# Optimization experiments

Measured on AMD Instinct MI355X. Metric: run time of the kernel, lower is better.

## Reference

```python
import jax, jax.numpy as jnp
import numpy as np

N_NODES = 100000
HIDDEN = 512
NUM_GRAPHS = 1024


def setup_inputs() -> dict:
    key = jax.random.key(0)
    k_h, k_b, k_w1, k_w2 = jax.random.split(key, 4)
    s1 = 1.0 / np.sqrt(HIDDEN)
    return {
        "h": jax.random.normal(k_h, (N_NODES, HIDDEN), dtype=jnp.float32),
        "batch_vec": jnp.sort(jax.random.randint(k_b, (N_NODES,), 0, NUM_GRAPHS, dtype=jnp.int32)),
        "W1": jax.random.normal(k_w1, (HIDDEN, HIDDEN), dtype=jnp.float32) * s1,
        "b1": jnp.zeros((HIDDEN,), dtype=jnp.float32),
        "W2": jax.random.normal(k_w2, (HIDDEN, 1), dtype=jnp.float32) * s1,
        "b2": jnp.zeros((1,), dtype=jnp.float32),
    }


def reference(h, batch_vec, W1, b1, W2, b2):
    # gate MLP (Dropout is identity in eval): [N, hidden] -> [N]
    gate = (jax.nn.gelu(h @ W1 + b1, approximate=False) @ W2 + b2)[:, 0]
    # segment softmax over graphs (batch_vec)
    m = jax.ops.segment_max(gate, batch_vec, num_segments=NUM_GRAPHS)
    e = jnp.exp(gate - m[batch_vec])
    denom = jax.ops.segment_sum(e, batch_vec, num_segments=NUM_GRAPHS)
    alpha = e / denom[batch_vec]  # [N]
    # scatter-weighted sum: [num_graphs, hidden]
    return jax.ops.segment_sum(alpha[:, None] * h, batch_vec, num_segments=NUM_GRAPHS)
```

## Files before the change

### kernel.cpp

```cpp
#include <hip/hip_runtime.h>
#include <hip/hip_bf16.h>
#include <float.h>

#define N_NODES 100000
#define HID     512
#define NGRAPH  1024
#define BM      48
#define NBLK    ((N_NODES + BM - 1) / BM)

typedef __bf16 bf16_t;
typedef bf16_t bf16x8 __attribute__((ext_vector_type(8)));
typedef float  f32x4  __attribute__((ext_vector_type(4)));

__device__ __forceinline__ float fast_gelu(float x) {
    const float z = __builtin_fabsf(x) * 0.70710678118654752f;
    const float t = __fdividef(1.0f, __builtin_fmaf(0.3275911f, z, 1.0f));
    float p = __builtin_fmaf(1.061405429f, t, -1.453152027f);
    p = __builtin_fmaf(p, t, 1.421413741f);
    p = __builtin_fmaf(p, t, -0.284496736f);
    p = __builtin_fmaf(p, t, 0.254829592f);
    p *= t;
    const float e    = __expf(-z * z);
    const float erfz = __builtin_fmaf(-p, e, 1.0f);
    const float s    = __builtin_copysignf(erfz, x);
    return 0.5f * x * (1.0f + s);
}

__global__ void __launch_bounds__(256) k_w1t_tiled(const float* __restrict__ w1,
                                                   bf16_t* __restrict__ bt) {
    const int u   = blockIdx.x * 256 + threadIdx.x;
    const int col = u & 511;
    const int g4  = u >> 9;
    const int k0  = g4 * 8;
    bf16x8 v;
    #pragma unroll
    for (int e = 0; e < 8; ++e)
        v[e] = (bf16_t)w1[(size_t)(k0 + e) * HID + col];
    *reinterpret_cast<bf16x8*>(bt + (size_t)u * 8) = v;
}

__global__ void __launch_bounds__(1024, 8) k_gemm_gate(const float* __restrict__ h,
                                                       const bf16_t* __restrict__ bt,
                                                       const float* __restrict__ b1,
                                                       const float* __restrict__ w2,
                                                       const float* __restrict__ b2,
                                                       float* __restrict__ gate) {
    __shared__ __align__(16) bf16_t As[BM * HID];
    __shared__ float gp[16][BM];

    const int tid  = threadIdx.x;
    const int lane = tid & 63;
    const int wv   = tid >> 6;
    const int l15  = lane & 15;
    const int l4   = lane >> 4;

    const int brow = blockIdx.x * BM;

    #pragma unroll
    for (int i = 0; i < 3; ++i) {
        const int idx = i * 1024 + tid;
        const int row = idx >> 6;
        const int cu  = idx & 63;
        const int grow = brow + row;
        f32x4 s0 = f32x4{0.f, 0.f, 0.f, 0.f}, s1 = s0;
        if (grow < N_NODES) {
            const f32x4* p = reinterpret_cast<const f32x4*>(
                h + (size_t)grow * HID + cu * 8);
            s0 = p[0];
            s1 = p[1];
        }
        bf16x8 v;
        #pragma unroll
        for (int j = 0; j < 4; ++j) { v[j] = (bf16_t)s0[j]; v[4 + j] = (bf16_t)s1[j]; }
        *reinterpret_cast<bf16x8*>(
            (char*)As + row * 1024 + ((cu ^ (row & 7)) * 16)) = v;
    }
    __syncthreads();

    const bf16_t* bbase = bt + ((size_t)l4 * 512 + wv * 32 + l15) * 8;
    const char*   abase = (const char*)As + l15 * 1024;
    f32x4 acc[3][2] = {};
    #pragma unroll 2
    for (int kt = 0; kt < 16; ++kt) {
        bf16x8 bfr[2];
        #pragma unroll
        for (int nf = 0; nf < 2; ++nf)
            bfr[nf] = *reinterpret_cast<const bf16x8*>(
                bbase + (size_t)kt * 16384 + nf * 128);
        const int chunkoff = ((kt * 4 + l4) ^ (l15 & 7)) * 16;
        bf16x8 af[3];
        #pragma unroll
        for (int mf = 0; mf < 3; ++mf)
            af[mf] = *reinterpret_cast<const bf16x8*>(abase + mf * 16384 + chunkoff);
        #pragma unroll
        for (int mf = 0; mf < 3; ++mf)
            #pragma unroll
            for (int nf = 0; nf < 2; ++nf)
                acc[mf][nf] = __builtin_amdgcn_mfma_f32_16x16x32_bf16(
                    af[mf], bfr[nf], acc[mf][nf], 0, 0, 0);
    }

    float pr[12];
    #pragma unroll
    for (int i = 0; i < 12; ++i) pr[i] = 0.f;
    #pragma unroll
    for (int nf = 0; nf < 2; ++nf) {
        const int cg    = wv * 32 + nf * 16 + l15;
        const float b1v = b1[cg];
        const float w2v = w2[cg];
        #pragma unroll
        for (int mf = 0; mf < 3; ++mf) {
            #pragma unroll
            for (int rr = 0; rr < 4; ++rr) {
                const float ge = fast_gelu(acc[mf][nf][rr] + b1v);
                pr[mf * 4 + rr] = fmaf(ge, w2v, pr[mf * 4 + rr]);
            }
        }
    }
    #pragma unroll
    for (int i = 0; i < 12; ++i) {
        float v = pr[i];
        v += __shfl_xor(v, 1);
        v += __shfl_xor(v, 2);
        v += __shfl_xor(v, 4);
        v += __shfl_xor(v, 8);
        pr[i] = v;
    }
    if (l15 == 0) {
        #pragma unroll
        for (int mf = 0; mf < 3; ++mf)
            #pragma unroll
            for (int rr = 0; rr < 4; ++rr)
                gp[wv][mf * 16 + l4 * 4 + rr] = pr[mf * 4 + rr];
    }
    __syncthreads();
    if (tid < BM) {
        const int grow = brow + tid;
        if (grow < N_NODES) {
            float s = b2[0];
            #pragma unroll
            for (int w = 0; w < 16; ++w) s += gp[w][tid];
            gate[grow] = s;
        }
    }
}

__global__ void __launch_bounds__(256) k_pool(const float* __restrict__ h,
                                              const int* __restrict__ bv,
                                              const float* __restrict__ gate,
                                              float* __restrict__ out) {
    const int g   = blockIdx.x;
    const int tid = threadIdx.x;
    __shared__ int   s_bounds[2];
    __shared__ float s_red[4];
    __shared__ float s_alpha[256];

    if (tid == 0) {
        int lo = 0, hi = N_NODES;
        while (lo < hi) { int mid = (lo + hi) >> 1; if (bv[mid] < g) lo = mid + 1; else hi = mid; }
        s_bounds[0] = lo;
        int lo2 = lo, hi2 = N_NODES;
        while (lo2 < hi2) { int mid = (lo2 + hi2) >> 1; if (bv[mid] < g + 1) lo2 = mid + 1; else hi2 = mid; }
        s_bounds[1] = lo2;
    }
    __syncthreads();
    const int start = s_bounds[0], end = s_bounds[1];

    float2 acc = make_float2(0.f, 0.f);
    if (start < end) {
        const int lane = tid & 63, wv = tid >> 6;
        float lm = -FLT_MAX;
        for (int i = start + tid; i < end; i += 256) lm = fmaxf(lm, gate[i]);
        #pragma unroll
        for (int o = 32; o; o >>= 1) lm = fmaxf(lm, __shfl_xor(lm, o));
        if (lane == 0) s_red[wv] = lm;
        __syncthreads();
        const float m = fmaxf(fmaxf(s_red[0], s_red[1]), fmaxf(s_red[2], s_red[3]));
        __syncthreads();
        float ls = 0.f;
        for (int i = start + tid; i < end; i += 256) ls += expf(gate[i] - m);
        #pragma unroll
        for (int o = 32; o; o >>= 1) ls += __shfl_xor(ls, o);
        if (lane == 0) s_red[wv] = ls;
        __syncthreads();
        const float inv = 1.f / (s_red[0] + s_red[1] + s_red[2] + s_red[3]);
        const float* hcol = h + tid * 2;
        for (int base = start; base < end; base += 256) {
            const int j = base + tid;
            const float av = (j < end) ? expf(gate[j] - m) * inv : 0.f;
            __syncthreads();
            s_alpha[tid] = av;
            __syncthreads();
            const int cnt = min(256, end - base);
            for (int jj = 0; jj < cnt; ++jj) {
                const float a = s_alpha[jj];
                const float2 hv = *reinterpret_cast<const float2*>(
                    hcol + (size_t)(base + jj) * HID);
                acc.x = fmaf(a, hv.x, acc.x);
                acc.y = fmaf(a, hv.y, acc.y);
            }
        }
    }
    *reinterpret_cast<float2*>(out + (size_t)g * HID + tid * 2) = acc;
}

extern "C" void kernel_launch(void* const* d_in, const int* in_sizes, int n_in,
                              void* d_out, int out_size, void* d_ws, size_t ws_size,
                              hipStream_t stream) {
    const float* h  = (const float*)d_in[0];
    const int*   bv = (const int*)d_in[1];
    const float* W1 = (const float*)d_in[2];
    const float* b1 = (const float*)d_in[3];
    const float* W2 = (const float*)d_in[4];
    const float* b2 = (const float*)d_in[5];
    float* out = (float*)d_out;

    char* ws = (char*)d_ws;
    bf16_t* bt   = (bf16_t*)ws;
    float*  gate = (float*)(ws + 524288);

    k_w1t_tiled<<<dim3(128), dim3(256), 0, stream>>>(W1, bt);
    k_gemm_gate<<<dim3(NBLK), dim3(1024), 0, stream>>>(h, bt, b1, W2, b2, gate);
    k_pool<<<dim3(NGRAPH), dim3(256), 0, stream>>>(h, bv, gate, out);
}
```

Measured before the change: 142.8 us.

## Make gate GEMM persistent with double-buffered LDS prefetch of next row block

The gate GEMM kernel now launches a fixed grid of 256 persistent blocks, each looping over row blocks. While computing the current block, it loads the next block of h into registers and writes it to a second LDS buffer, and it software-pipelines the W1 fragment loads two k-steps ahead. This aims to hide global-memory latency behind MFMA work and to drop the per-block startup cost. In exchange it doubles LDS use (two 48 KB buffers, so launch bounds drop to 4), raises register pressure, and with 256 blocks on the MI355X may leave CUs underfilled.

```diff
diff --git a/kernel.cpp b/kernel.cpp
--- a/kernel.cpp
+++ b/kernel.cpp
@@ -6,7 +6,8 @@
 #define HID     512
 #define NGRAPH  1024
 #define BM      48
-#define NBLK    ((N_NODES + BM - 1) / BM)
+#define NRB     ((N_NODES + BM - 1) / BM)
+#define GRID    256
 
 typedef __bf16 bf16_t;
 typedef bf16_t bf16x8 __attribute__((ext_vector_type(8)));
@@ -39,13 +40,13 @@
     *reinterpret_cast<bf16x8*>(bt + (size_t)u * 8) = v;
 }
 
-__global__ void __launch_bounds__(1024, 8) k_gemm_gate(const float* __restrict__ h,
+__global__ void __launch_bounds__(1024, 4) k_gemm_gate(const float* __restrict__ h,
                                                        const bf16_t* __restrict__ bt,
                                                        const float* __restrict__ b1,
                                                        const float* __restrict__ w2,
                                                        const float* __restrict__ b2,
                                                        float* __restrict__ gate) {
-    __shared__ __align__(16) bf16_t As[BM * HID];
+    __shared__ __align__(16) bf16_t As[2][BM * HID];
     __shared__ float gp[16][BM];
 
     const int tid  = threadIdx.x;
@@ -54,94 +55,150 @@
     const int l15  = lane & 15;
     const int l4   = lane >> 4;
 
-    const int brow = blockIdx.x * BM;
-
-    #pragma unroll
-    for (int i = 0; i < 3; ++i) {
-        const int idx = i * 1024 + tid;
-        const int row = idx >> 6;
-        const int cu  = idx & 63;
-        const int grow = brow + row;
-        f32x4 s0 = f32x4{0.f, 0.f, 0.f, 0.f}, s1 = s0;
-        if (grow < N_NODES) {
-            const f32x4* p = reinterpret_cast<const f32x4*>(
-                h + (size_t)grow * HID + cu * 8);
-            s0 = p[0];
-            s1 = p[1];
-        }
-        bf16x8 v;
-        #pragma unroll
-        for (int j = 0; j < 4; ++j) { v[j] = (bf16_t)s0[j]; v[4 + j] = (bf16_t)s1[j]; }
-        *reinterpret_cast<bf16x8*>(
-            (char*)As + row * 1024 + ((cu ^ (row & 7)) * 16)) = v;
-    }
-    __syncthreads();
-
-    const bf16_t* bbase = bt + ((size_t)l4 * 512 + wv * 32 + l15) * 8;
-    const char*   abase = (const char*)As + l15 * 1024;
-    f32x4 acc[3][2] = {};
-    #pragma unroll 2
-    for (int kt = 0; kt < 16; ++kt) {
-        bf16x8 bfr[2];
-        #pragma unroll
-        for (int nf = 0; nf < 2; ++nf)
-            bfr[nf] = *reinterpret_cast<const bf16x8*>(
-                bbase + (size_t)kt * 16384 + nf * 128);
-        const int chunkoff = ((kt * 4 + l4) ^ (l15 & 7)) * 16;
-        bf16x8 af[3];
-        #pragma unroll
-        for (int mf = 0; mf < 3; ++mf)
-            af[mf] = *reinterpret_cast<const bf16x8*>(abase + mf * 16384 + chunkoff);
-        #pragma unroll
-        for (int mf = 0; mf < 3; ++mf)
-            #pragma unroll
-            for (int nf = 0; nf < 2; ++nf)
-                acc[mf][nf] = __builtin_amdgcn_mfma_f32_16x16x32_bf16(
-                    af[mf], bfr[nf], acc[mf][nf], 0, 0, 0);
-    }
-
-    float pr[12];
-    #pragma unroll
-    for (int i = 0; i < 12; ++i) pr[i] = 0.f;
+    float b1v[2], w2v[2];
     #pragma unroll
     for (int nf = 0; nf < 2; ++nf) {
-        const int cg    = wv * 32 + nf * 16 + l15;
-        const float b1v = b1[cg];
-        const float w2v = w2[cg];
-        #pragma unroll
-        for (int mf = 0; mf < 3; ++mf) {
-            #pragma unroll
-            for (int rr = 0; rr < 4; ++rr) {
-                const float ge = fast_gelu(acc[mf][nf][rr] + b1v);
-                pr[mf * 4 + rr] = fmaf(ge, w2v, pr[mf * 4 + rr]);
-            }
-        }
-    }
-    #pragma unroll
-    for (int i = 0; i < 12; ++i) {
-        float v = pr[i];
-        v += __shfl_xor(v, 1);
-        v += __shfl_xor(v, 2);
-        v += __shfl_xor(v, 4);
-        v += __shfl_xor(v, 8);
-        pr[i] = v;
-    }
-    if (l15 == 0) {
-        #pragma unroll
-        for (int mf = 0; mf < 3; ++mf)
-            #pragma unroll
-            for (int rr = 0; rr < 4; ++rr)
-                gp[wv][mf * 16 + l4 * 4 + rr] = pr[mf * 4 + rr];
+        const int cg = wv * 32 + nf * 16 + l15;
+        b1v[nf] = b1[cg];
+        w2v[nf] = w2[cg];
+    }
+    const float b2v = b2[0];
+
+    const bf16_t* bbase = bt + ((size_t)l4 * 512 + wv * 32 + l15) * 8;
+
+    {
+        const int rb = blockIdx.x;
+        #pragma unroll
+        for (int i = 0; i < 3; ++i) {
+            const int idx = i * 1024 + tid;
+            const int row = idx >> 6;
+            const int cu  = idx & 63;
+            const int grow = rb * BM + row;
+            f32x4 s0 = f32x4{0.f, 0.f, 0.f, 0.f}, s1 = s0;
+            if (grow < N_NODES) {
+                const f32x4* p = reinterpret_cast<const f32x4*>(
+                    h + (size_t)grow * HID + cu * 8);
+                s0 = p[0]; s1 = p[1];
+            }
+            bf16x8 v;
+            #pragma unroll
+            for (int j = 0; j < 4; ++j) { v[j] = (bf16_t)s0[j]; v[4 + j] = (bf16_t)s1[j]; }
+            *reinterpret_cast<bf16x8*>(
+                (char*)&As[0][0] + row * 1024 + ((cu ^ (row & 7)) * 16)) = v;
+        }
     }
     __syncthreads();
-    if (tid < BM) {
-        const int grow = brow + tid;
-        if (grow < N_NODES) {
-            float s = b2[0];
-            #pragma unroll
-            for (int w = 0; w < 16; ++w) s += gp[w][tid];
-            gate[grow] = s;
-        }
+
+    int cur = 0;
+    for (int rb = blockIdx.x; rb < NRB; rb += GRID) {
+        const int  rbn  = rb + GRID;
+        const bool have = rbn < NRB;
+
+        f32x4 st[6];
+        if (have) {
+            #pragma unroll
+            for (int i = 0; i < 3; ++i) {
+                const int idx = i * 1024 + tid;
+                const int row = idx >> 6;
+                const int cu  = idx & 63;
+                const int grow = rbn * BM + row;
+                f32x4 s0 = f32x4{0.f, 0.f, 0.f, 0.f}, s1 = s0;
+                if (grow < N_NODES) {
+                    const f32x4* p = reinterpret_cast<const f32x4*>(
+                        h + (size_t)grow * HID + cu * 8);
+                    s0 = p[0]; s1 = p[1];
+                }
+                st[2 * i] = s0; st[2 * i + 1] = s1;
+            }
+        }
+
+        const char* abase = (const char*)&As[cur][0] + l15 * 1024;
+        f32x4 acc[3][2] = {};
+        bf16x8 breg[2][2];
+        #pragma unroll
+        for (int nf = 0; nf < 2; ++nf)
+            breg[0][nf] = *reinterpret_cast<const bf16x8*>(bbase + nf * 128);
+        #pragma unroll
+        for (int nf = 0; nf < 2; ++nf)
+            breg[1][nf] = *reinterpret_cast<const bf16x8*>(bbase + 16384 + nf * 128);
+        #pragma unroll 4
+        for (int kt = 0; kt < 16; ++kt) {
+            const int chunkoff = ((kt * 4 + l4) ^ (l15 & 7)) * 16;
+            bf16x8 af[3];
+            #pragma unroll
+            for (int mf = 0; mf < 3; ++mf)
+                af[mf] = *reinterpret_cast<const bf16x8*>(
+                    abase + mf * 16384 + chunkoff);
+            #pragma unroll
+            for (int mf = 0; mf < 3; ++mf)
+                #pragma unroll
+                for (int nf = 0; nf < 2; ++nf)
+                    acc[mf][nf] = __builtin_amdgcn_mfma_f32_16x16x32_bf16(
+                        af[mf], breg[kt & 1][nf], acc[mf][nf], 0, 0, 0);
+            if (kt < 14) {
+                #pragma unroll
+                for (int nf = 0; nf < 2; ++nf)
+                    breg[kt & 1][nf] = *reinterpret_cast<const bf16x8*>(
+                        bbase + (size_t)(kt + 2) * 16384 + nf * 128);
+            }
+        }
+
+        if (have) {
+            #pragma unroll
+            for (int i = 0; i < 3; ++i) {
+                const int idx = i * 1024 + tid;
+                const int row = idx >> 6;
+                const int cu  = idx & 63;
+                bf16x8 v;
+                #pragma unroll
+                for (int j = 0; j < 4; ++j) { v[j] = (bf16_t)st[2*i][j]; v[4+j] = (bf16_t)st[2*i+1][j]; }
+                *reinterpret_cast<bf16x8*>(
+                    (char*)&As[cur ^ 1][0] + row * 1024 + ((cu ^ (row & 7)) * 16)) = v;
+            }
+        }
+
+        float pr[12];
+        #pragma unroll
+        for (int i = 0; i < 12; ++i) pr[i] = 0.f;
+        #pragma unroll
+        for (int nf = 0; nf < 2; ++nf) {
+            #pragma unroll
+            for (int mf = 0; mf < 3; ++mf) {
+                #pragma unroll
+                for (int rr = 0; rr < 4; ++rr) {
+                    const float ge = fast_gelu(acc[mf][nf][rr] + b1v[nf]);
+                    pr[mf * 4 + rr] = fmaf(ge, w2v[nf], pr[mf * 4 + rr]);
+                }
+            }
+        }
+        #pragma unroll
+        for (int i = 0; i < 12; ++i) {
+            float v = pr[i];
+            v += __shfl_xor(v, 1);
+            v += __shfl_xor(v, 2);
+            v += __shfl_xor(v, 4);
+            v += __shfl_xor(v, 8);
+            pr[i] = v;
+        }
+        __syncthreads();
+        if (l15 == 0) {
+            #pragma unroll
+            for (int mf = 0; mf < 3; ++mf)
+                #pragma unroll
+                for (int rr = 0; rr < 4; ++rr)
+                    gp[wv][mf * 16 + l4 * 4 + rr] = pr[mf * 4 + rr];
+        }
+        __syncthreads();
+        if (tid < BM) {
+            const int grow = rb * BM + tid;
+            if (grow < N_NODES) {
+                float s = b2v;
+                #pragma unroll
+                for (int w = 0; w < 16; ++w) s += gp[w][tid];
+                gate[grow] = s;
+            }
+        }
+        cur ^= 1;
     }
 }
 
@@ -220,6 +277,6 @@
     float*  gate = (float*)(ws + 524288);
 
     k_w1t_tiled<<<dim3(128), dim3(256), 0, stream>>>(W1, bt);
-    k_gemm_gate<<<dim3(NBLK), dim3(1024), 0, stream>>>(h, bt, b1, W2, b2, gate);
+    k_gemm_gate<<<dim3(GRID), dim3(1024), 0, stream>>>(h, bt, b1, W2, b2, gate);
     k_pool<<<dim3(NGRAPH), dim3(256), 0, stream>>>(h, bv, gate, out);
 }
```

Result: slower. 151.6 us (+6.2%).
